# Kernel tuning notes

Hardware: AMD Instinct MI355X
Metric: run time of the kernel (lower is better)

Reference implementation:

```python
import jax, jax.numpy as jnp
import numpy as np

QMIN, QMAX = -128.0, 127.0


def setup_inputs() -> dict:
    key = jax.random.key(0)
    k1, k2, k3 = jax.random.split(key, 3)
    x = jax.random.normal(k1, (8, 32, 32, 32), jnp.float32)          # NCHW
    weight = jax.random.normal(k2, (32, 32, 3, 3), jnp.float32) * 0.1  # OIHW
    bias = jax.random.normal(k3, (32,), jnp.float32) * 0.01
    # lut[i, j] = (i - 128) * (j - 128), indexed by (q + 128).
    i = jnp.arange(256, dtype=jnp.float32) - 128.0
    lut = i[:, None] * i[None, :]
    return {"x": x, "weight": weight, "bias": bias, "lut": lut}


def reference(x, weight, bias, lut):
    # dynamic per-tensor scales (qmethod = ('dynamic','tensor','tensor'))
    sf = jax.lax.stop_gradient(jnp.max(jnp.abs(x)) / 127.0)
    sw = jax.lax.stop_gradient(jnp.max(jnp.abs(weight)) / 127.0)

    qx = jnp.clip(jnp.round(x / sf), QMIN, QMAX)        # int8 values as float
    qw = jnp.clip(jnp.round(weight / sw), QMIN, QMAX)

    # STE fake-quant tensors (forward = dequant, backward = identity)
    x_fq = x + jax.lax.stop_gradient(qx * sf - x)
    w_fq = weight + jax.lax.stop_gradient(qw * sw - weight)

    pad = ((1, 1), (1, 1))
    conv_fq = jax.lax.conv_general_dilated(
        x_fq, w_fq, window_strides=(1, 1), padding=pad,
        dimension_numbers=('NCHW', 'OIHW', 'NCHW'))

    # ---- LUT-based int8 conv path (forward value) ----
    # im2col on the int8 activation codes; zero padding -> q=0 -> index 128,
    # and lut[128, :] == 0, matching zero-padded conv.
    patches = jax.lax.conv_general_dilated_patches(
        qx, filter_shape=(3, 3), window_strides=(1, 1), padding=pad)
    N, K, Hp, Wp = patches.shape                       # K = Cin*kh*kw
    O = qw.shape[0]
    ix = (patches + 128.0).astype(jnp.int32).reshape(N, K, Hp * Wp)
    ix = jnp.transpose(ix, (0, 2, 1))                  # [N, P, K]
    iw = (qw.reshape(O, K) + 128.0).astype(jnp.int32)  # [O, K]

    # gather approximate products and accumulate over the window
    prods = lut[ix[:, :, None, :], iw[None, None, :, :]]  # [N, P, O, K]
    out_lut = (sf * sw) * jnp.sum(prods, axis=-1)          # [N, P, O]
    out_lut = jnp.transpose(out_lut, (0, 2, 1)).reshape(N, O, Hp, Wp)

    b = bias[None, :, None, None]
    out_fq = conv_fq + b
    out_lut = out_lut + b
    # forward returns the LUT result; gradients flow through the fake-quant conv (STE)
    return out_fq + jax.lax.stop_gradient(out_lut - out_fq)
```

## Files before the change

### kernel.cpp

```cpp
#include <hip/hip_runtime.h>

#define MAGIC 0x5A17C0DEu

static __device__ __forceinline__ int dot4(int a, int b, int acc) {
#if defined(__has_builtin)
#if __has_builtin(__builtin_amdgcn_sdot4)
  return __builtin_amdgcn_sdot4(a, b, acc, false);
#define DOT4_DONE 1
#endif
#endif
#ifndef DOT4_DONE
  #pragma unroll
  for (int k = 0; k < 4; k++)
    acc += ((a >> (8*k)) << 24 >> 24) * ((b >> (8*k)) << 24 >> 24);
  return acc;
#endif
}

__global__ __launch_bounds__(256) void k_one(
    const float* __restrict__ x, const float* __restrict__ w,
    const float* __restrict__ bias, float* __restrict__ out,
    unsigned long long* __restrict__ tags) {
  __shared__ float redp[4];
  __shared__ float s_sf;
  __shared__ __align__(16) int qw_lds[2304];
  __shared__ __align__(16) int qxt[4][34][8];

  int b = blockIdx.x, t = threadIdx.x;

  if (b < 64) {
    const float4* x4 = (const float4*)x;
    float m = 0.f;
    #pragma unroll
    for (int k = 0; k < 4; k++) {
      float4 v = x4[b * 1024 + k * 256 + t];
      m = fmaxf(m, fmaxf(fmaxf(fabsf(v.x), fabsf(v.y)), fmaxf(fabsf(v.z), fabsf(v.w))));
    }
    #pragma unroll
    for (int s = 1; s < 64; s <<= 1) m = fmaxf(m, __shfl_xor(m, s, 64));
    if ((t & 63) == 0) redp[t >> 6] = m;
    __syncthreads();
    if (t == 0) {
      float mm = fmaxf(fmaxf(redp[0], redp[1]), fmaxf(redp[2], redp[3]));
      unsigned long long v =
          ((unsigned long long)MAGIC << 32) | (unsigned long long)__float_as_uint(mm);
      __hip_atomic_store(&tags[b], v, __ATOMIC_RELEASE, __HIP_MEMORY_SCOPE_AGENT);
    }
    return;
  }

  int b2 = b - 64;
  int n = b2 >> 5, hpair = (b2 >> 1) & 15, ohalf = b2 & 1;
  int h0 = hpair * 2;
  int wlane = t & 31, g = t >> 5;

  float xv[4][4];
  #pragma unroll
  for (int r = 0; r < 4; r++) {
    int y = h0 - 1 + r;
    bool valid = (y >= 0) && (y < 32);
    #pragma unroll
    for (int j = 0; j < 4; j++)
      xv[r][j] = valid ? x[n * 32768 + (g * 4 + j) * 1024 + y * 32 + wlane] : 0.f;
  }

  float mw = 0.f;
  #pragma unroll
  for (int j = 0; j < 9; j++) {
    float4 u = ((const float4*)w)[t + 256 * j];
    mw = fmaxf(mw, fmaxf(fmaxf(fabsf(u.x), fabsf(u.y)), fmaxf(fabsf(u.z), fabsf(u.w))));
  }
  #pragma unroll
  for (int s = 1; s < 64; s <<= 1) mw = fmaxf(mw, __shfl_xor(mw, s, 64));
  if ((t & 63) == 0) redp[t >> 6] = mw;
  __syncthreads();
  float sw = fmaxf(fmaxf(redp[0], redp[1]), fmaxf(redp[2], redp[3])) / 127.f;

  signed char* qw8 = (signed char*)qw_lds;
  #pragma unroll
  for (int j = 0; j < 36; j++) {
    int i = t + 256 * j;
    int o = i / 288, rem = i % 288;
    int c = rem / 9, k9 = rem % 9;
    float r = rintf(w[i] / sw);
    r = fminf(fmaxf(r, -128.f), 127.f);
    qw8[(o * 9 + k9) * 32 + c] = (signed char)(int)r;
  }

  if (t < 64) {
    unsigned long long v;
    for (;;) {
      v = __hip_atomic_load(&tags[t], __ATOMIC_ACQUIRE, __HIP_MEMORY_SCOPE_AGENT);
      if ((unsigned)(v >> 32) == MAGIC) break;
      __builtin_amdgcn_s_sleep(1);
    }
    float pm = __uint_as_float((unsigned)v);
    #pragma unroll
    for (int s = 1; s < 64; s <<= 1) pm = fmaxf(pm, __shfl_xor(pm, s, 64));
    if (t == 0) s_sf = pm / 127.f;
  }
  __syncthreads();
  float inv_sf = 1.f / s_sf;
  float scale = s_sf * sw;

  #pragma unroll
  for (int r = 0; r < 4; r++) {
    int packed = 0;
    #pragma unroll
    for (int j = 0; j < 4; j++) {
      float rr = fminf(fmaxf(rintf(xv[r][j] * inv_sf), -128.f), 127.f);
      packed |= ((int)rr & 0xff) << (8 * j);
    }
    qxt[r][wlane + 1][g] = packed;
  }
  if (t < 64) {
    int r = t >> 4, col = ((t >> 3) & 1) * 33, g2 = t & 7;
    qxt[r][col][g2] = 0;
  }
  __syncthreads();

  int wv = t >> 6, l = t & 63;
  int hs = l >> 5, ww = l & 31;
  int h = h0 + hs;

  int4 p[3][6];
  #pragma unroll
  for (int r = 0; r < 3; r++) {
    const int4* row = (const int4*)(&qxt[hs + r][ww][0]);
    #pragma unroll
    for (int k = 0; k < 6; k++) p[r][k] = row[k];
  }

  #pragma unroll
  for (int j = 0; j < 4; j++) {
    int o = ohalf * 16 + wv * 4 + j;
    const int* wr = qw_lds + o * 72;
    int acc = 0;
    #pragma unroll
    for (int ky = 0; ky < 3; ky++) {
      const int* wk = wr + ky * 24;
      #pragma unroll
      for (int k = 0; k < 6; k++) {
        const int4 pp = p[ky][k];
        acc = dot4(pp.x, wk[k * 4 + 0], acc);
        acc = dot4(pp.y, wk[k * 4 + 1], acc);
        acc = dot4(pp.z, wk[k * 4 + 2], acc);
        acc = dot4(pp.w, wk[k * 4 + 3], acc);
      }
    }
    out[(n * 32 + o) * 1024 + h * 32 + ww] = scale * (float)acc + bias[o];
  }
}

extern "C" void kernel_launch(void* const* d_in, const int* in_sizes, int n_in,
                              void* d_out, int out_size, void* d_ws, size_t ws_size,
                              hipStream_t stream) {
  (void)in_sizes; (void)n_in; (void)out_size; (void)ws_size;
  const float* x    = (const float*)d_in[0];
  const float* w    = (const float*)d_in[1];
  const float* bias = (const float*)d_in[2];
  float* out = (float*)d_out;

  unsigned long long* tags = (unsigned long long*)d_ws;

  k_one<<<320, 256, 0, stream>>>(x, w, bias, out, tags);
}
```

Measured before the change: 66.96 us.

## Fold activation max-reduction into compute blocks and drop dedicated reducer blocks

The 64 blocks that only computed the global max|x| are removed. Each of the 256 compute blocks now takes per-wave maxima from the x rows it already loads and publishes them as tagged atomics. Every block then polls all 1024 tags to build the scale. This avoids reading x a second time and launching extra blocks. In exchange each block does more polling and reduction, and correctness now depends on all 256 blocks being resident at the same time.

New measurement: 101.6 us. 1.52x slower.

```diff
diff --git a/kernel.cpp b/kernel.cpp
--- a/kernel.cpp
+++ b/kernel.cpp
@@ -1,6 +1,6 @@
 #include <hip/hip_runtime.h>
 
-#define MAGIC 0x5A17C0DEu
+#define MAGIC 0x5A17C0DEull
 
 static __device__ __forceinline__ int dot4(int a, int b, int acc) {
 #if defined(__has_builtin)
@@ -22,46 +22,34 @@
     const float* __restrict__ bias, float* __restrict__ out,
     unsigned long long* __restrict__ tags) {
   __shared__ float redp[4];
-  __shared__ float s_sf;
   __shared__ __align__(16) int qw_lds[2304];
   __shared__ __align__(16) int qxt[4][34][8];
 
   int b = blockIdx.x, t = threadIdx.x;
-
-  if (b < 64) {
-    const float4* x4 = (const float4*)x;
-    float m = 0.f;
-    #pragma unroll
-    for (int k = 0; k < 4; k++) {
-      float4 v = x4[b * 1024 + k * 256 + t];
-      m = fmaxf(m, fmaxf(fmaxf(fabsf(v.x), fabsf(v.y)), fmaxf(fabsf(v.z), fabsf(v.w))));
-    }
-    #pragma unroll
-    for (int s = 1; s < 64; s <<= 1) m = fmaxf(m, __shfl_xor(m, s, 64));
-    if ((t & 63) == 0) redp[t >> 6] = m;
-    __syncthreads();
-    if (t == 0) {
-      float mm = fmaxf(fmaxf(redp[0], redp[1]), fmaxf(redp[2], redp[3]));
-      unsigned long long v =
-          ((unsigned long long)MAGIC << 32) | (unsigned long long)__float_as_uint(mm);
-      __hip_atomic_store(&tags[b], v, __ATOMIC_RELEASE, __HIP_MEMORY_SCOPE_AGENT);
-    }
-    return;
-  }
-
-  int b2 = b - 64;
-  int n = b2 >> 5, hpair = (b2 >> 1) & 15, ohalf = b2 & 1;
+  int n = b >> 5, hpair = (b >> 1) & 15, ohalf = b & 1;
   int h0 = hpair * 2;
   int wlane = t & 31, g = t >> 5;
+  int wv = t >> 6;
 
   float xv[4][4];
+  float mx = 0.f;
   #pragma unroll
   for (int r = 0; r < 4; r++) {
     int y = h0 - 1 + r;
     bool valid = (y >= 0) && (y < 32);
     #pragma unroll
-    for (int j = 0; j < 4; j++)
-      xv[r][j] = valid ? x[n * 32768 + (g * 4 + j) * 1024 + y * 32 + wlane] : 0.f;
+    for (int j = 0; j < 4; j++) {
+      float vv = valid ? x[n * 32768 + (g * 4 + j) * 1024 + y * 32 + wlane] : 0.f;
+      xv[r][j] = vv;
+      mx = fmaxf(mx, fabsf(vv));
+    }
+  }
+  #pragma unroll
+  for (int s = 1; s < 64; s <<= 1) mx = fmaxf(mx, __shfl_xor(mx, s, 64));
+  if ((t & 63) == 0) {
+    unsigned long long v = (MAGIC << 32) | (unsigned long long)__float_as_uint(mx);
+    __hip_atomic_store(&tags[b * 4 + wv], v, __ATOMIC_RELEASE,
+                       __HIP_MEMORY_SCOPE_AGENT);
   }
 
   float mw = 0.f;
@@ -72,7 +60,7 @@
   }
   #pragma unroll
   for (int s = 1; s < 64; s <<= 1) mw = fmaxf(mw, __shfl_xor(mw, s, 64));
-  if ((t & 63) == 0) redp[t >> 6] = mw;
+  if ((t & 63) == 0) redp[wv] = mw;
   __syncthreads();
   float sw = fmaxf(fmaxf(redp[0], redp[1]), fmaxf(redp[2], redp[3])) / 127.f;
 
@@ -86,22 +74,27 @@
     r = fminf(fmaxf(r, -128.f), 127.f);
     qw8[(o * 9 + k9) * 32 + c] = (signed char)(int)r;
   }
+  __syncthreads();
 
-  if (t < 64) {
+  float pm = 0.f;
+  #pragma unroll
+  for (int k = 0; k < 4; k++) {
     unsigned long long v;
     for (;;) {
-      v = __hip_atomic_load(&tags[t], __ATOMIC_ACQUIRE, __HIP_MEMORY_SCOPE_AGENT);
-      if ((unsigned)(v >> 32) == MAGIC) break;
+      v = __hip_atomic_load(&tags[t + 256 * k], __ATOMIC_ACQUIRE,
+                            __HIP_MEMORY_SCOPE_AGENT);
+      if ((unsigned)(v >> 32) == (unsigned)MAGIC) break;
       __builtin_amdgcn_s_sleep(1);
     }
-    float pm = __uint_as_float((unsigned)v);
-    #pragma unroll
-    for (int s = 1; s < 64; s <<= 1) pm = fmaxf(pm, __shfl_xor(pm, s, 64));
-    if (t == 0) s_sf = pm / 127.f;
+    pm = fmaxf(pm, __uint_as_float((unsigned)v));
   }
+  #pragma unroll
+  for (int s = 1; s < 64; s <<= 1) pm = fmaxf(pm, __shfl_xor(pm, s, 64));
+  if ((t & 63) == 0) redp[wv] = pm;
   __syncthreads();
-  float inv_sf = 1.f / s_sf;
-  float scale = s_sf * sw;
+  float sf = fmaxf(fmaxf(redp[0], redp[1]), fmaxf(redp[2], redp[3])) / 127.f;
+  float inv_sf = 1.f / sf;
+  float scale = sf * sw;
 
   #pragma unroll
   for (int r = 0; r < 4; r++) {
@@ -119,7 +112,7 @@
   }
   __syncthreads();
 
-  int wv = t >> 6, l = t & 63;
+  int l = t & 63;
   int hs = l >> 5, ww = l & 31;
   int h = h0 + hs;
 
@@ -163,5 +156,5 @@
 
   unsigned long long* tags = (unsigned long long*)d_ws;
 
-  k_one<<<320, 256, 0, stream>>>(x, w, bias, out, tags);
+  k_one<<<256, 256, 0, stream>>>(x, w, bias, out, tags);
 }
```
